# Optimization experiments

Hardware: AMD Instinct MI355X
Metric: run time of the kernel (lower is better)

The kernel has to match this reference:

```python
import jax, jax.numpy as jnp
import numpy as np

D_MODEL = 1024
N_HEADS = 16
HEAD_DIM = D_MODEL // N_HEADS
NEG_INF = -1e10


def setup_inputs() -> dict:
    key = jax.random.key(0)
    ks = jax.random.split(key, 6)
    B, S = 2, 2048
    x = jax.random.normal(ks[0], (B, S, D_MODEL), dtype=jnp.float32)
    mask = jnp.ones((B, S), dtype=jnp.int32)
    scale_w = 1.0 / np.sqrt(D_MODEL)
    Wq = jax.random.normal(ks[1], (D_MODEL, D_MODEL), dtype=jnp.float32) * scale_w
    Wk = jax.random.normal(ks[2], (D_MODEL, D_MODEL), dtype=jnp.float32) * scale_w
    Wv = jax.random.normal(ks[3], (D_MODEL, D_MODEL), dtype=jnp.float32) * scale_w
    Wo = jax.random.normal(ks[4], (D_MODEL, D_MODEL), dtype=jnp.float32) * scale_w
    bq = jnp.zeros((D_MODEL,), jnp.float32)
    bk = jnp.zeros((D_MODEL,), jnp.float32)
    bv = jnp.zeros((D_MODEL,), jnp.float32)
    bo = jnp.zeros((D_MODEL,), jnp.float32)
    return {"x": x, "mask": mask, "Wq": Wq, "bq": bq, "Wk": Wk, "bk": bk,
            "Wv": Wv, "bv": bv, "Wo": Wo, "bo": bo}


def reference(x, mask, Wq, bq, Wk, bk, Wv, bv, Wo, bo):
    B, S, _ = x.shape
    # Linear projections (torch Linear: y = x @ W.T + b)
    Q = x @ Wq.T + bq
    K = x @ Wk.T + bk
    V = x @ Wv.T + bv
    # [B, H, S, Dh]
    Q = Q.reshape(B, S, N_HEADS, HEAD_DIM).transpose(0, 2, 1, 3)
    K = K.reshape(B, S, N_HEADS, HEAD_DIM).transpose(0, 2, 1, 3)
    V = V.reshape(B, S, N_HEADS, HEAD_DIM).transpose(0, 2, 1, 3)
    scale = jnp.sqrt(jnp.float32(HEAD_DIM))
    energy = jnp.einsum('bhqd,bhkd->bhqk', Q, K) / scale  # [B,H,S,S]
    # mask: [B,S] -> broadcast over heads and query dim (keys masked)
    m = mask[:, None, None, :]  # [B,1,1,S]
    energy = jnp.where(m == 0, jnp.float32(NEG_INF), energy)
    attention = jax.nn.softmax(energy, axis=-1)
    # dropout in eval mode = identity
    out = jnp.einsum('bhqk,bhkd->bhqd', attention, V)  # [B,H,S,Dh]
    out = out.transpose(0, 2, 1, 3).reshape(B, S, D_MODEL)
    return out @ Wo.T + bo
```

## Files before the change

kernel.cpp:

```cpp
#include <hip/hip_runtime.h>
#include <hip/hip_bf16.h>

typedef __hip_bfloat16 bf16;
typedef __attribute__((ext_vector_type(8))) short s8v;
typedef __attribute__((ext_vector_type(4))) float f4v;

#define D_MODEL 1024
#define S_LEN   2048
#define BATCH   2
#define NH      16
#define HD      64
#define M_TOTAL 4096

__device__ __forceinline__ void gll16(const bf16* g, bf16* l) {
    __builtin_amdgcn_global_load_lds(
        (const __attribute__((address_space(1))) void*)g,
        (__attribute__((address_space(3))) void*)l, 16, 0, 0);
}

__global__ __launch_bounds__(256) void cvt_bf16x8(const float* __restrict__ s,
                                                  bf16* __restrict__ d, int n) {
    int i = (blockIdx.x * 256 + threadIdx.x) * 8;
    if (i < n) {
        float4 a = *(const float4*)(s + i);
        float4 b = *(const float4*)(s + i + 4);
        union { bf16 h[8]; uint4 u; } p;
        p.h[0] = __float2bfloat16(a.x); p.h[1] = __float2bfloat16(a.y);
        p.h[2] = __float2bfloat16(a.z); p.h[3] = __float2bfloat16(a.w);
        p.h[4] = __float2bfloat16(b.x); p.h[5] = __float2bfloat16(b.y);
        p.h[6] = __float2bfloat16(b.z); p.h[7] = __float2bfloat16(b.w);
        *(uint4*)(d + i) = p.u;
    }
}

struct WPtrs { const float* s0; const float* s1; const float* s2; const float* s3;
               bf16* d0; bf16* d1; bf16* d2; bf16* d3; };

__global__ __launch_bounds__(256) void cvt_w(WPtrs p) {
    const float* s; bf16* d;
    switch (blockIdx.y) {
        case 0:  s = p.s0; d = p.d0; break;
        case 1:  s = p.s1; d = p.d1; break;
        case 2:  s = p.s2; d = p.d2; break;
        default: s = p.s3; d = p.d3; break;
    }
    int i = (blockIdx.x * 256 + threadIdx.x) * 8;
    float4 a = *(const float4*)(s + i);
    float4 b = *(const float4*)(s + i + 4);
    union { bf16 h[8]; uint4 u; } q;
    q.h[0] = __float2bfloat16(a.x); q.h[1] = __float2bfloat16(a.y);
    q.h[2] = __float2bfloat16(a.z); q.h[3] = __float2bfloat16(a.w);
    q.h[4] = __float2bfloat16(b.x); q.h[5] = __float2bfloat16(b.y);
    q.h[6] = __float2bfloat16(b.z); q.h[7] = __float2bfloat16(b.w);
    *(uint4*)(d + i) = q.u;
}

template<int TM, int TN>
__device__ __forceinline__ void gemm_main(const bf16* __restrict__ A,
                                          const bf16* __restrict__ W,
                                          bf16* As, bf16* Bs,
                                          int bm, int bn,
                                          f4v (&acc)[TM/32][TN/32])
{
    constexpr int FM = TM / 32, FN = TN / 32;
    constexpr int CALLS_A = TM / 16, CALLS = (TM + TN) / 16, PW = CALLS / 4;
    const int t = threadIdx.x, wv = t >> 6, lane = t & 63;
    const int quad = lane >> 4, l15 = lane & 15;
    const int wm = (wv >> 1) * (TM / 2), wn = (wv & 1) * (TN / 2);
    const int lr = lane >> 2, lc = (lane & 3) * 8;

    const bf16* aptr[FM];
    const bf16* bptr[FN];
    #pragma unroll
    for (int i = 0; i < FM; ++i) aptr[i] = As + (wm + i * 16 + l15) * 32 + quad * 8;
    #pragma unroll
    for (int j = 0; j < FN; ++j) bptr[j] = Bs + (wn + j * 16 + l15) * 32 + quad * 8;

    for (int k0 = 0; k0 < D_MODEL; k0 += 32) {
        __syncthreads();
        #pragma unroll
        for (int c = 0; c < PW; ++c) {
            const int cc = wv * PW + c;
            if (cc < CALLS_A) {
                gll16(A + (size_t)(bm + cc * 16 + lr) * D_MODEL + k0 + lc,
                      As + cc * 16 * 32);
            } else {
                const int r2 = cc - CALLS_A;
                gll16(W + (size_t)(bn + r2 * 16 + lr) * D_MODEL + k0 + lc,
                      Bs + r2 * 16 * 32);
            }
        }
        __syncthreads();

        s8v af[FM], bfv[FN];
        #pragma unroll
        for (int i = 0; i < FM; ++i) af[i] = *(const s8v*)aptr[i];
        #pragma unroll
        for (int j = 0; j < FN; ++j) bfv[j] = *(const s8v*)bptr[j];
        #pragma unroll
        for (int i = 0; i < FM; ++i)
            #pragma unroll
            for (int j = 0; j < FN; ++j)
                acc[i][j] = __builtin_amdgcn_mfma_f32_16x16x32_bf16(af[i], bfv[j], acc[i][j], 0, 0, 0);
    }
}

__global__ __launch_bounds__(256) void gemm_qkv(
    const bf16* __restrict__ x,
    const bf16* __restrict__ Wq, const bf16* __restrict__ Wk, const bf16* __restrict__ Wv,
    const float* __restrict__ bq, const float* __restrict__ bk, const float* __restrict__ bv,
    bf16* __restrict__ Qb, bf16* __restrict__ Kb, bf16* __restrict__ Vtb)
{
    __shared__ __align__(16) bf16 As[128 * 32];
    __shared__ __align__(16) bf16 Bs[128 * 32];
    __shared__ __align__(16) bf16 Tw[4][64][72];
    const int z = blockIdx.z;
    const bf16*  W    = (z == 0) ? Wq : (z == 1) ? Wk : Wv;
    const float* bias = (z == 0) ? bq : (z == 1) ? bk : bv;
    bf16*        out  = (z == 0) ? Qb : (z == 1) ? Kb : Vtb;
    const int bm = blockIdx.y * 128, bn = blockIdx.x * 128;

    f4v acc[4][4] = {};
    gemm_main<128, 128>(x, W, As, Bs, bm, bn, acc);

    const int t = threadIdx.x, wv = t >> 6, lane = t & 63;
    const int quad = lane >> 4, l15 = lane & 15;
    const int wm = (wv >> 1) * 64, wn = (wv & 1) * 64;

    if (z == 2) {
        #pragma unroll
        for (int j = 0; j < 4; ++j) {
            const int col = bn + wn + j * 16 + l15;
            const float bv_ = bias[col];
            #pragma unroll
            for (int i = 0; i < 4; ++i) {
                #pragma unroll
                for (int rp = 0; rp < 4; rp += 2) {
                    union { bf16 h[2]; unsigned u; } p2;
                    p2.h[0] = __float2bfloat16(acc[i][j][rp]     + bv_);
                    p2.h[1] = __float2bfloat16(acc[i][j][rp + 1] + bv_);
                    *(unsigned*)&Tw[wv][j * 16 + l15][i * 16 + quad * 4 + rp] = p2.u;
                }
            }
        }
        const int bb = (bm + wm) >> 11, s0 = (bm + wm) & 2047;
        #pragma unroll
        for (int p = 0; p < 8; ++p) {
            const int dl = p * 8 + (lane >> 3);
            const int sl = (lane & 7) * 8;
            const int col = bn + wn + dl;
            const int h = col >> 6, d = col & 63;
            uint4 v = *(const uint4*)&Tw[wv][dl][sl];
            *(uint4*)&out[(((size_t)(bb * NH + h)) * HD + d) * S_LEN + s0 + sl] = v;
        }
    } else {
        #pragma unroll
        for (int j = 0; j < 4; ++j) {
            const int col = bn + wn + j * 16 + l15;
            const float bv_ = bias[col];
            const int h = col >> 6, d = col & 63;
            #pragma unroll
            for (int i = 0; i < 4; ++i) {
                #pragma unroll
                for (int r = 0; r < 4; ++r) {
                    const int row = bm + wm + i * 16 + quad * 4 + r;
                    const int b = row >> 11, s = row & 2047;
                    const float v = acc[i][j][r] + bv_;
                    out[(((size_t)(b * NH + h)) * S_LEN + s) * HD + d] = __float2bfloat16(v);
                }
            }
        }
    }
}

__global__ __launch_bounds__(256) void gemm_out(
    const bf16* __restrict__ Ob, const bf16* __restrict__ Wo,
    const float* __restrict__ bo, float* __restrict__ out)
{
    __shared__ __align__(16) bf16 As[64 * 32];
    __shared__ __align__(16) bf16 Bs[128 * 32];
    const int bm = blockIdx.y * 64, bn = blockIdx.x * 128;

    f4v acc[2][4] = {};
    gemm_main<64, 128>(Ob, Wo, As, Bs, bm, bn, acc);

    const int t = threadIdx.x, wv = t >> 6, lane = t & 63;
    const int quad = lane >> 4, l15 = lane & 15;
    const int wm = (wv >> 1) * 32, wn = (wv & 1) * 64;
    #pragma unroll
    for (int j = 0; j < 4; ++j) {
        const int col = bn + wn + j * 16 + l15;
        const float bv_ = bo[col];
        #pragma unroll
        for (int i = 0; i < 2; ++i)
            #pragma unroll
            for (int r = 0; r < 4; ++r) {
                const int row = bm + wm + i * 16 + quad * 4 + r;
                out[(size_t)row * D_MODEL + col] = acc[i][j][r] + bv_;
            }
    }
}

__global__ __launch_bounds__(256) void attn_mfma(
    const bf16* __restrict__ Q, const bf16* __restrict__ K,
    const bf16* __restrict__ Vt, const int* __restrict__ mask,
    bf16* __restrict__ O)
{
    __shared__ __align__(16) bf16 Ks[64][72];
    __shared__ __align__(16) bf16 Vts[64][72];
    __shared__ __align__(16) bf16 Ps[4][16][72];
    __shared__ float mb[64];

    const int t = threadIdx.x, wv = t >> 6, lane = t & 63;
    const int quad = lane >> 4, l15 = lane & 15;
    const int qt = blockIdx.x & 31, h = (blockIdx.x >> 5) & 15, b = blockIdx.x >> 9;
    const int q0 = qt * 64;
    const size_t qkbase = ((size_t)(b * NH + h)) * S_LEN * HD;
    const size_t vtbase = ((size_t)(b * NH + h)) * HD * S_LEN;

    const float KSC  = 0.125f * 1.44269504f;
    const float THR2 = 8.0f * 1.44269504f;

    const bf16* qrow = Q + qkbase + (size_t)(q0 + wv * 16 + l15) * HD;
    const s8v qf0 = *(const s8v*)(qrow + quad * 8);
    const s8v qf1 = *(const s8v*)(qrow + 32 + quad * 8);

    const int srow = t >> 2, scoff = (t & 3) * 16;

    uint4 kr0, kr1, vr0, vr1; int mr = 1;
    auto LOADT = [&](int kt2) {
        const int kk = kt2 * 64;
        const uint4* kp = (const uint4*)(K  + qkbase + (size_t)(kk + srow) * HD + scoff);
        const uint4* vp = (const uint4*)(Vt + vtbase + (size_t)srow * S_LEN + kk + scoff);
        kr0 = kp[0]; kr1 = kp[1];
        vr0 = vp[0]; vr1 = vp[1];
        if (t < 64) mr = mask[b * S_LEN + kk + t];
    };
    LOADT(0);

    float mprev = -1e30f, lsum = 0.f;
    f4v oacc[4] = {};

    for (int kt = 0; kt < S_LEN / 64; ++kt) {
        __syncthreads();
        *(uint4*)&Ks[srow][scoff]       = kr0;
        *(uint4*)&Ks[srow][scoff + 8]   = kr1;
        *(uint4*)&Vts[srow][scoff]      = vr0;
        *(uint4*)&Vts[srow][scoff + 8]  = vr1;
        if (t < 64) mb[t] = mr ? 0.f : -1e30f;
        __syncthreads();
        if (kt + 1 < S_LEN / 64) LOADT(kt + 1);

        f4v st[4];
        __builtin_amdgcn_s_setprio(1);
        #pragma unroll
        for (int c = 0; c < 4; ++c) {
            s8v kf0 = *(const s8v*)&Ks[c * 16 + l15][quad * 8];
            s8v kf1 = *(const s8v*)&Ks[c * 16 + l15][32 + quad * 8];
            f4v z = {0.f, 0.f, 0.f, 0.f};
            z = __builtin_amdgcn_mfma_f32_16x16x32_bf16(kf0, qf0, z, 0, 0, 0);
            z = __builtin_amdgcn_mfma_f32_16x16x32_bf16(kf1, qf1, z, 0, 0, 0);
            st[c] = z;
        }
        __builtin_amdgcn_s_setprio(0);

        float mt = -1e30f;
        #pragma unroll
        for (int c = 0; c < 4; ++c) {
            const float4 mk = *(const float4*)&mb[c * 16 + quad * 4];
            const float v0 = st[c][0] * KSC + mk.x;
            const float v1 = st[c][1] * KSC + mk.y;
            const float v2 = st[c][2] * KSC + mk.z;
            const float v3 = st[c][3] * KSC + mk.w;
            st[c][0] = v0; st[c][1] = v1; st[c][2] = v2; st[c][3] = v3;
            mt = fmaxf(mt, fmaxf(fmaxf(v0, v1), fmaxf(v2, v3)));
        }
        mt = fmaxf(mt, __shfl_xor(mt, 16, 64));
        mt = fmaxf(mt, __shfl_xor(mt, 32, 64));

        float mn = mprev;
        if (!__all(mt <= mprev + THR2)) {
            mn = fmaxf(mprev, mt);
            const float alpha = __builtin_amdgcn_exp2f(mprev - mn);
            mprev = mn;
            float av[4];
            #pragma unroll
            for (int r = 0; r < 4; ++r) av[r] = __shfl(alpha, quad * 4 + r, 64);
            #pragma unroll
            for (int dt = 0; dt < 4; ++dt)
                #pragma unroll
                for (int r = 0; r < 4; ++r) oacc[dt][r] *= av[r];
            lsum *= alpha;
        }

        float ps = 0.f;
        #pragma unroll
        for (int c = 0; c < 4; ++c) {
            #pragma unroll
            for (int r = 0; r < 4; ++r) {
                const float p = __builtin_amdgcn_exp2f(st[c][r] - mn);
                st[c][r] = p;
                ps += p;
            }
        }
        lsum += ps;

        #pragma unroll
        for (int c = 0; c < 4; ++c) {
            union { bf16 h[4]; short4 s4; } pk;
            pk.h[0] = __float2bfloat16(st[c][0]);
            pk.h[1] = __float2bfloat16(st[c][1]);
            pk.h[2] = __float2bfloat16(st[c][2]);
            pk.h[3] = __float2bfloat16(st[c][3]);
            *(short4*)&Ps[wv][l15][c * 16 + quad * 4] = pk.s4;
        }

        s8v pf0 = *(const s8v*)&Ps[wv][l15][quad * 8];
        s8v pf1 = *(const s8v*)&Ps[wv][l15][32 + quad * 8];
        __builtin_amdgcn_s_setprio(1);
        #pragma unroll
        for (int dt = 0; dt < 4; ++dt) {
            s8v vf0 = *(const s8v*)&Vts[dt * 16 + l15][quad * 8];
            s8v vf1 = *(const s8v*)&Vts[dt * 16 + l15][32 + quad * 8];
            oacc[dt] = __builtin_amdgcn_mfma_f32_16x16x32_bf16(pf0, vf0, oacc[dt], 0, 0, 0);
            oacc[dt] = __builtin_amdgcn_mfma_f32_16x16x32_bf16(pf1, vf1, oacc[dt], 0, 0, 0);
        }
        __builtin_amdgcn_s_setprio(0);
    }

    lsum += __shfl_xor(lsum, 16, 64);
    lsum += __shfl_xor(lsum, 32, 64);
    float linv[4];
    #pragma unroll
    for (int r = 0; r < 4; ++r) linv[r] = 1.f / __shfl(lsum, quad * 4 + r, 64);
    #pragma unroll
    for (int dt = 0; dt < 4; ++dt) {
        #pragma unroll
        for (int r = 0; r < 4; ++r) {
            const int s = q0 + wv * 16 + quad * 4 + r;
            const int col = h * 64 + dt * 16 + l15;
            O[((size_t)b * S_LEN + s) * D_MODEL + col] = __float2bfloat16(oacc[dt][r] * linv[r]);
        }
    }
}

extern "C" void kernel_launch(void* const* d_in, const int* in_sizes, int n_in,
                              void* d_out, int out_size, void* d_ws, size_t ws_size,
                              hipStream_t stream) {
    const float* x    = (const float*)d_in[0];
    const int*   mask = (const int*)  d_in[1];
    const float* Wq   = (const float*)d_in[2];
    const float* bq   = (const float*)d_in[3];
    const float* Wk   = (const float*)d_in[4];
    const float* bk   = (const float*)d_in[5];
    const float* Wv   = (const float*)d_in[6];
    const float* bv   = (const float*)d_in[7];
    const float* Wo   = (const float*)d_in[8];
    const float* bo   = (const float*)d_in[9];
    float* out = (float*)d_out;

    char* w = (char*)d_ws;
    bf16* xb  = (bf16*)w; w += (size_t)M_TOTAL * D_MODEL * 2;
    bf16* Wqb = (bf16*)w; w += (size_t)D_MODEL * D_MODEL * 2;
    bf16* Wkb = (bf16*)w; w += (size_t)D_MODEL * D_MODEL * 2;
    bf16* Wvb = (bf16*)w; w += (size_t)D_MODEL * D_MODEL * 2;
    bf16* Wob = (bf16*)w; w += (size_t)D_MODEL * D_MODEL * 2;
    bf16* Qb  = (bf16*)w; w += (size_t)M_TOTAL * D_MODEL * 2;
    bf16* Kb  = (bf16*)w; w += (size_t)M_TOTAL * D_MODEL * 2;
    bf16* Vtb = (bf16*)w; w += (size_t)M_TOTAL * D_MODEL * 2;
    bf16* Ob  = (bf16*)w; w += (size_t)M_TOTAL * D_MODEL * 2;

    const int nx = M_TOTAL * D_MODEL;
    cvt_bf16x8<<<nx / 2048, 256, 0, stream>>>(x, xb, nx);
    WPtrs wp = { Wq, Wk, Wv, Wo, Wqb, Wkb, Wvb, Wob };
    cvt_w<<<dim3(D_MODEL * D_MODEL / 2048, 4), 256, 0, stream>>>(wp);

    gemm_qkv<<<dim3(8, 32, 3), 256, 0, stream>>>(xb, Wqb, Wkb, Wvb, bq, bk, bv, Qb, Kb, Vtb);

    attn_mfma<<<BATCH * NH * (S_LEN / 64), 256, 0, stream>>>(Qb, Kb, Vtb, mask, Ob);

    gemm_out<<<dim3(8, 64), 256, 0, stream>>>(Ob, Wob, bo, out);
}
```

Baseline: 233.2 us.

## Double-buffer GEMM and attention tiles via async global-to-LDS loads with XOR swizzle

Converts the GEMM main loop and the attention K/V loop to double-buffered LDS staging, using global_load_lds to prefetch the next tile while MFMAs run on the current one, with one barrier per iteration. Attention tiles switch from padded rows to an XOR-swizzled unpadded layout to avoid bank conflicts. The mask is read directly from global memory instead of LDS, and blocks are reordered so batch and head vary fastest. The QKV kernel aliases its transpose buffer onto the GEMM staging memory to keep LDS use down, which needs an extra barrier and correct swizzle indexing.

```diff
diff --git a/kernel.cpp b/kernel.cpp
--- a/kernel.cpp
+++ b/kernel.cpp
@@ -11,6 +11,7 @@
 #define NH      16
 #define HD      64
 #define M_TOTAL 4096
+#define NT      (S_LEN / 64)
 
 __device__ __forceinline__ void gll16(const bf16* g, bf16* l) {
     __builtin_amdgcn_global_load_lds(
@@ -69,39 +70,47 @@
     const int wm = (wv >> 1) * (TM / 2), wn = (wv & 1) * (TN / 2);
     const int lr = lane >> 2, lc = (lane & 3) * 8;
 
-    const bf16* aptr[FM];
-    const bf16* bptr[FN];
-    #pragma unroll
-    for (int i = 0; i < FM; ++i) aptr[i] = As + (wm + i * 16 + l15) * 32 + quad * 8;
-    #pragma unroll
-    for (int j = 0; j < FN; ++j) bptr[j] = Bs + (wn + j * 16 + l15) * 32 + quad * 8;
-
-    for (int k0 = 0; k0 < D_MODEL; k0 += 32) {
-        __syncthreads();
+    auto STAGE = [&](int buf, int k0) {
         #pragma unroll
         for (int c = 0; c < PW; ++c) {
             const int cc = wv * PW + c;
             if (cc < CALLS_A) {
                 gll16(A + (size_t)(bm + cc * 16 + lr) * D_MODEL + k0 + lc,
-                      As + cc * 16 * 32);
+                      As + buf * (TM * 32) + cc * 16 * 32);
             } else {
                 const int r2 = cc - CALLS_A;
                 gll16(W + (size_t)(bn + r2 * 16 + lr) * D_MODEL + k0 + lc,
-                      Bs + r2 * 16 * 32);
+                      Bs + buf * (TN * 32) + r2 * 16 * 32);
             }
         }
-        __syncthreads();
-
+    };
+
+    STAGE(0, 0);
+    __syncthreads();
+    int cur = 0;
+
+    for (int k0 = 0; k0 < D_MODEL; k0 += 32) {
+        if (k0 + 32 < D_MODEL) STAGE(cur ^ 1, k0 + 32);
+
+        const bf16* ab = As + cur * (TM * 32);
+        const bf16* bb = Bs + cur * (TN * 32);
         s8v af[FM], bfv[FN];
         #pragma unroll
-        for (int i = 0; i < FM; ++i) af[i] = *(const s8v*)aptr[i];
-        #pragma unroll
-        for (int j = 0; j < FN; ++j) bfv[j] = *(const s8v*)bptr[j];
+        for (int i = 0; i < FM; ++i)
+            af[i] = *(const s8v*)(ab + (wm + i * 16 + l15) * 32 + quad * 8);
+        #pragma unroll
+        for (int j = 0; j < FN; ++j)
+            bfv[j] = *(const s8v*)(bb + (wn + j * 16 + l15) * 32 + quad * 8);
+        __builtin_amdgcn_s_setprio(1);
         #pragma unroll
         for (int i = 0; i < FM; ++i)
             #pragma unroll
             for (int j = 0; j < FN; ++j)
                 acc[i][j] = __builtin_amdgcn_mfma_f32_16x16x32_bf16(af[i], bfv[j], acc[i][j], 0, 0, 0);
+        __builtin_amdgcn_s_setprio(0);
+
+        __syncthreads();
+        cur ^= 1;
     }
 }
 
@@ -111,9 +120,11 @@
     const float* __restrict__ bq, const float* __restrict__ bk, const float* __restrict__ bv,
     bf16* __restrict__ Qb, bf16* __restrict__ Kb, bf16* __restrict__ Vtb)
 {
-    __shared__ __align__(16) bf16 As[128 * 32];
-    __shared__ __align__(16) bf16 Bs[128 * 32];
-    __shared__ __align__(16) bf16 Tw[4][64][72];
+    __shared__ __align__(16) char smem[4 * 64 * 72 * 2];
+    bf16* As = (bf16*)smem;
+    bf16* Bs = (bf16*)(smem + 2 * 128 * 32 * 2);
+    bf16 (*Tw)[64][72] = (bf16(*)[64][72])smem;
+
     const int z = blockIdx.z;
     const bf16*  W    = (z == 0) ? Wq : (z == 1) ? Wk : Wv;
     const float* bias = (z == 0) ? bq : (z == 1) ? bk : bv;
@@ -128,6 +139,7 @@
     const int wm = (wv >> 1) * 64, wn = (wv & 1) * 64;
 
     if (z == 2) {
+        __syncthreads();
         #pragma unroll
         for (int j = 0; j < 4; ++j) {
             const int col = bn + wn + j * 16 + l15;
@@ -177,12 +189,12 @@
     const bf16* __restrict__ Ob, const bf16* __restrict__ Wo,
     const float* __restrict__ bo, float* __restrict__ out)
 {
-    __shared__ __align__(16) bf16 As[64 * 32];
-    __shared__ __align__(16) bf16 Bs[128 * 32];
+    __shared__ __align__(16) bf16 As[2][64 * 32];
+    __shared__ __align__(16) bf16 Bs[2][128 * 32];
     const int bm = blockIdx.y * 64, bn = blockIdx.x * 128;
 
     f4v acc[2][4] = {};
-    gemm_main<64, 128>(Ob, Wo, As, Bs, bm, bn, acc);
+    gemm_main<64, 128>(Ob, Wo, &As[0][0], &Bs[0][0], bm, bn, acc);
 
     const int t = threadIdx.x, wv = t >> 6, lane = t & 63;
     const int quad = lane >> 4, l15 = lane & 15;
@@ -206,14 +218,15 @@
     const bf16* __restrict__ Vt, const int* __restrict__ mask,
     bf16* __restrict__ O)
 {
-    __shared__ __align__(16) bf16 Ks[64][72];
-    __shared__ __align__(16) bf16 Vts[64][72];
-    __shared__ __align__(16) bf16 Ps[4][16][72];
-    __shared__ float mb[64];
+    __shared__ __align__(16) bf16 Ks[2][64][64];
+    __shared__ __align__(16) bf16 Vts[2][64][64];
+    __shared__ __align__(16) bf16 Ps[4][16][64];
 
     const int t = threadIdx.x, wv = t >> 6, lane = t & 63;
     const int quad = lane >> 4, l15 = lane & 15;
-    const int qt = blockIdx.x & 31, h = (blockIdx.x >> 5) & 15, b = blockIdx.x >> 9;
+    const int sw = l15 & 7;
+    const int bid = blockIdx.x;
+    const int b = bid & 1, h = (bid >> 1) & 15, qt = bid >> 5;
     const int q0 = qt * 64;
     const size_t qkbase = ((size_t)(b * NH + h)) * S_LEN * HD;
     const size_t vtbase = ((size_t)(b * NH + h)) * HD * S_LEN;
@@ -225,38 +238,46 @@
     const s8v qf0 = *(const s8v*)(qrow + quad * 8);
     const s8v qf1 = *(const s8v*)(qrow + 32 + quad * 8);
 
-    const int srow = t >> 2, scoff = (t & 3) * 16;
-
-    uint4 kr0, kr1, vr0, vr1; int mr = 1;
-    auto LOADT = [&](int kt2) {
-        const int kk = kt2 * 64;
-        const uint4* kp = (const uint4*)(K  + qkbase + (size_t)(kk + srow) * HD + scoff);
-        const uint4* vp = (const uint4*)(Vt + vtbase + (size_t)srow * S_LEN + kk + scoff);
-        kr0 = kp[0]; kr1 = kp[1];
-        vr0 = vp[0]; vr1 = vp[1];
-        if (t < 64) mr = mask[b * S_LEN + kk + t];
+    const int grl = lane >> 3, gch = (lane & 7) ^ grl;
+    auto STAGEKV = [&](int bf, int kt2) {
+        const int k0s = kt2 * 64;
+        #pragma unroll
+        for (int g = 0; g < 2; ++g) {
+            const int r0 = wv * 16 + g * 8;
+            gll16(K  + qkbase + (size_t)(k0s + r0 + grl) * HD + gch * 8,
+                  &Ks[bf][r0][0]);
+            gll16(Vt + vtbase + (size_t)(r0 + grl) * S_LEN + k0s + gch * 8,
+                  &Vts[bf][r0][0]);
+        }
     };
-    LOADT(0);
+
+    STAGEKV(0, 0);
+    __syncthreads();
 
     float mprev = -1e30f, lsum = 0.f;
     f4v oacc[4] = {};
-
-    for (int kt = 0; kt < S_LEN / 64; ++kt) {
-        __syncthreads();
-        *(uint4*)&Ks[srow][scoff]       = kr0;
-        *(uint4*)&Ks[srow][scoff + 8]   = kr1;
-        *(uint4*)&Vts[srow][scoff]      = vr0;
-        *(uint4*)&Vts[srow][scoff + 8]  = vr1;
-        if (t < 64) mb[t] = mr ? 0.f : -1e30f;
-        __syncthreads();
-        if (kt + 1 < S_LEN / 64) LOADT(kt + 1);
+    int cur = 0;
+
+    for (int kt = 0; kt < NT; ++kt) {
+        const int k0 = kt * 64;
+        const bool more = (kt + 1 < NT);
+        if (more) STAGEKV(cur ^ 1, kt + 1);
+
+        int4 mk[4];
+        #pragma unroll
+        for (int c = 0; c < 4; ++c)
+            mk[c] = *(const int4*)&mask[b * S_LEN + k0 + c * 16 + quad * 4];
+
+        const char* kbase = (const char*)&Ks[cur][0][0];
+        const char* vbase = (const char*)&Vts[cur][0][0];
 
         f4v st[4];
         __builtin_amdgcn_s_setprio(1);
         #pragma unroll
         for (int c = 0; c < 4; ++c) {
-            s8v kf0 = *(const s8v*)&Ks[c * 16 + l15][quad * 8];
-            s8v kf1 = *(const s8v*)&Ks[c * 16 + l15][32 + quad * 8];
+            const char* kr = kbase + (c * 16 + l15) * 128;
+            s8v kf0 = *(const s8v*)(kr + ((quad ^ sw) << 4));
+            s8v kf1 = *(const s8v*)(kr + (((4 + quad) ^ sw) << 4));
             f4v z = {0.f, 0.f, 0.f, 0.f};
             z = __builtin_amdgcn_mfma_f32_16x16x32_bf16(kf0, qf0, z, 0, 0, 0);
             z = __builtin_amdgcn_mfma_f32_16x16x32_bf16(kf1, qf1, z, 0, 0, 0);
@@ -267,13 +288,13 @@
         float mt = -1e30f;
         #pragma unroll
         for (int c = 0; c < 4; ++c) {
-            const float4 mk = *(const float4*)&mb[c * 16 + quad * 4];
-            const float v0 = st[c][0] * KSC + mk.x;
-            const float v1 = st[c][1] * KSC + mk.y;
-            const float v2 = st[c][2] * KSC + mk.z;
-            const float v3 = st[c][3] * KSC + mk.w;
-            st[c][0] = v0; st[c][1] = v1; st[c][2] = v2; st[c][3] = v3;
-            mt = fmaxf(mt, fmaxf(fmaxf(v0, v1), fmaxf(v2, v3)));
+            f4v m4;
+            m4[0] = mk[c].x ? 0.f : -1e30f;
+            m4[1] = mk[c].y ? 0.f : -1e30f;
+            m4[2] = mk[c].z ? 0.f : -1e30f;
+            m4[3] = mk[c].w ? 0.f : -1e30f;
+            st[c] = st[c] * KSC + m4;
+            mt = fmaxf(mt, fmaxf(fmaxf(st[c][0], st[c][1]), fmaxf(st[c][2], st[c][3])));
         }
         mt = fmaxf(mt, __shfl_xor(mt, 16, 64));
         mt = fmaxf(mt, __shfl_xor(mt, 32, 64));
@@ -293,39 +314,46 @@
             lsum *= alpha;
         }
 
-        float ps = 0.f;
+        f4v psv = {0.f, 0.f, 0.f, 0.f};
         #pragma unroll
         for (int c = 0; c < 4; ++c) {
-            #pragma unroll
-            for (int r = 0; r < 4; ++r) {
-                const float p = __builtin_amdgcn_exp2f(st[c][r] - mn);
-                st[c][r] = p;
-                ps += p;
-            }
-        }
-        lsum += ps;
-
+            f4v e = st[c] - mn;
+            e[0] = __builtin_amdgcn_exp2f(e[0]);
+            e[1] = __builtin_amdgcn_exp2f(e[1]);
+            e[2] = __builtin_amdgcn_exp2f(e[2]);
+            e[3] = __builtin_amdgcn_exp2f(e[3]);
+            st[c] = e;
+            psv += e;
+        }
+        lsum += psv[0] + psv[1] + psv[2] + psv[3];
+
+        char* pr = (char*)&Ps[wv][l15][0];
         #pragma unroll
         for (int c = 0; c < 4; ++c) {
-            union { bf16 h[4]; short4 s4; } pk;
-            pk.h[0] = __float2bfloat16(st[c][0]);
-            pk.h[1] = __float2bfloat16(st[c][1]);
-            pk.h[2] = __float2bfloat16(st[c][2]);
-            pk.h[3] = __float2bfloat16(st[c][3]);
-            *(short4*)&Ps[wv][l15][c * 16 + quad * 4] = pk.s4;
-        }
-
-        s8v pf0 = *(const s8v*)&Ps[wv][l15][quad * 8];
-        s8v pf1 = *(const s8v*)&Ps[wv][l15][32 + quad * 8];
+            union { bf16 hh[4]; short4 s4; } pk;
+            pk.hh[0] = __float2bfloat16(st[c][0]);
+            pk.hh[1] = __float2bfloat16(st[c][1]);
+            pk.hh[2] = __float2bfloat16(st[c][2]);
+            pk.hh[3] = __float2bfloat16(st[c][3]);
+            const int wch = (2 * c + (quad >> 1)) ^ sw;
+            *(short4*)(pr + (wch << 4) + ((quad & 1) << 3)) = pk.s4;
+        }
+        s8v pf0 = *(const s8v*)(pr + ((quad ^ sw) << 4));
+        s8v pf1 = *(const s8v*)(pr + (((4 + quad) ^ sw) << 4));
+
         __builtin_amdgcn_s_setprio(1);
         #pragma unroll
         for (int dt = 0; dt < 4; ++dt) {
-            s8v vf0 = *(const s8v*)&Vts[dt * 16 + l15][quad * 8];
-            s8v vf1 = *(const s8v*)&Vts[dt * 16 + l15][32 + quad * 8];
+            const char* vr = vbase + (dt * 16 + l15) * 128;
+            s8v vf0 = *(const s8v*)(vr + ((quad ^ sw) << 4));
+            s8v vf1 = *(const s8v*)(vr + (((4 + quad) ^ sw) << 4));
             oacc[dt] = __builtin_amdgcn_mfma_f32_16x16x32_bf16(pf0, vf0, oacc[dt], 0, 0, 0);
             oacc[dt] = __builtin_amdgcn_mfma_f32_16x16x32_bf16(pf1, vf1, oacc[dt], 0, 0, 0);
         }
         __builtin_amdgcn_s_setprio(0);
+
+        if (more) __syncthreads();
+        cur ^= 1;
     }
 
     lsum += __shfl_xor(lsum, 16, 64);
```

Result: slower. 241.6 us (+3.6%).
